# Kernel tuning notes

Hardware: AMD Instinct MI355X
Metric: run time of the kernel (lower is better)

Reference implementation:

```python
import jax, jax.numpy as jnp
import numpy as np

# Module constants (from source defaults)
RING = 256      # ring_len
D = 128         # slot_dim
IN = 64         # input_dim
SD = max(8, D // 3)  # sensory_dim = 42
K = 2           # gauss_k -> 2K+1 = 5 taps
TAU = 8.0       # gauss_tau
NC = 1000       # num_classes
B, T = 512, 512


def setup_inputs() -> dict:
    key = jax.random.key(0)
    ks = jax.random.split(key, 10)
    g = lambda k, shape, s=0.05: jax.random.normal(k, shape, jnp.float32) * s
    return {
        "x": jax.random.normal(ks[0], (B, T, IN), jnp.float32),
        "theta_ptr": jnp.array([37.0], jnp.float32),
        "w_proj": g(ks[1], (SD, IN)), "b_proj": jnp.zeros((SD,), jnp.float32),
        "w_ih": g(ks[2], (3 * SD, SD)), "w_hh": g(ks[3], (3 * SD, SD)),
        "b_ih": jnp.zeros((3 * SD,), jnp.float32), "b_hh": jnp.zeros((3 * SD,), jnp.float32),
        "w_bridge": g(ks[4], (D, SD)), "b_bridge": jnp.zeros((D,), jnp.float32),
        "w_jump": g(ks[5], (1, D)), "b_jump": jnp.zeros((1,), jnp.float32),
        "w_gate": g(ks[6], (1, D)), "b_gate": jnp.zeros((1,), jnp.float32),
        "w_cls": g(ks[7], (NC, D)), "b_cls": jnp.zeros((NC,), jnp.float32),
    }


def _kernel(ptr):
    """Gaussian soft window around a fractional ring pointer. ptr: [B] float."""
    offs = jnp.arange(-K, K + 1)
    base = jnp.floor(ptr)
    frac = ptr - base                               # [B]
    pos = jnp.mod(base.astype(jnp.int32)[:, None] + offs[None, :], RING)  # [B, 2K+1]
    d = offs.astype(ptr.dtype)[None, :] - frac[:, None]
    w = jax.nn.softmax(-(d * d) / TAU, axis=-1)     # [B, 2K+1]
    return pos, w


def reference(x, theta_ptr, w_proj, b_proj, w_ih, w_hh, b_ih, b_hh,
              w_bridge, b_bridge, w_jump, b_jump, w_gate, b_gate, w_cls, b_cls):
    Bn = x.shape[0]
    bidx = jnp.arange(Bn)
    ring0 = jnp.zeros((Bn, RING, D), x.dtype)
    h0 = jnp.zeros((Bn, SD), x.dtype)
    ptr0 = jnp.broadcast_to(jnp.mod(theta_ptr, float(RING)), (Bn,)).astype(x.dtype)

    def step(carry, xt):
        ring, h, ptr = carry
        # sensory path: Linear -> GRUCell -> bridge
        s = xt @ w_proj.T + b_proj
        gx = s @ w_ih.T + b_ih
        gh = h @ w_hh.T + b_hh
        rg = jax.nn.sigmoid(gx[:, :SD] + gh[:, :SD])
        zg = jax.nn.sigmoid(gx[:, SD:2 * SD] + gh[:, SD:2 * SD])
        ng = jnp.tanh(gx[:, 2 * SD:] + rg * gh[:, 2 * SD:])
        h = (1.0 - zg) * ng + zg * h
        u = jnp.tanh(h @ w_bridge.T + b_bridge)      # write vector [B, D]
        # soft-kernel read at current pointer
        pos, w = _kernel(ptr)
        r = jnp.einsum('bk,bkd->bd', w, ring[bidx[:, None], pos])
        # pointer jump target + gate, circ_lerp along shortest arc
        jump = jax.nn.sigmoid(r @ w_jump.T + b_jump)[:, 0] * RING
        gate = jax.nn.sigmoid(r @ w_gate.T + b_gate)[:, 0]
        delta = jnp.mod(jump - ptr + RING / 2.0, float(RING)) - RING / 2.0  # wrap_delta
        ptr = jnp.mod(ptr + gate * delta, float(RING))                      # circ_lerp
        # soft-kernel write at new pointer
        pos2, w2 = _kernel(ptr)
        ring = ring.at[bidx[:, None], pos2].add(w2[..., None] * u[:, None, :])
        return (ring, h, ptr), None

    (ring, h, ptr), _ = jax.lax.scan(step, (ring0, h0, ptr0), jnp.swapaxes(x, 0, 1))
    pos, w = _kernel(ptr)
    r = jnp.einsum('bk,bkd->bd', w, ring[bidx[:, None], pos])
    return r @ w_cls.T + b_cls
```

## Files before the change

### kernel.cpp

```cpp
#include <hip/hip_runtime.h>
#include <hip/hip_bf16.h>
#include <cstdint>

#define RINGN 256
#define DD    128
#define SDN   42
#define G3N   126
#define INN   64
#define BN    512
#define TN    512
#define NCN   1000
#define HS    44
#define GXS   128
#define BT    (BN * TN)
#define HSLOTS 32
#define GSLOTS 16

typedef float v2f __attribute__((ext_vector_type(2)));
typedef float4 __attribute__((may_alias)) f4ma;
typedef float2 __attribute__((may_alias)) f2ma;

__device__ __forceinline__ float sigm(float x)    { return 1.0f / (1.0f + __expf(-x)); }
__device__ __forceinline__ float tanhfast(float x){ float e = __expf(2.0f * x); return 1.0f - 2.0f / (e + 1.0f); }
__device__ __forceinline__ float wrap256(float x) { return x - 256.0f * floorf(x * 0.00390625f); }

__device__ __forceinline__ void taps_norm(float p, int* pos, float* w) {
  float base = floorf(p);
  float frac = p - base;
  int ib = (int)base;
  float e[5];
  float s = 0.0f;
#pragma unroll
  for (int k = 0; k < 5; k++) {
    float d = (float)(k - 2) - frac;
    e[k] = __expf(-(d * d) * 0.125f);
    s += e[k];
    pos[k] = (ib + k - 2) & 255;
  }
  float inv = 1.0f / s;
#pragma unroll
  for (int k = 0; k < 5; k++) w[k] = e[k] * inv;
}

template<int C>
__device__ __forceinline__ float dpp_add_step(float x) {
  int t = __builtin_amdgcn_update_dpp(0, __float_as_int(x), C, 0xf, 0xf, true);
  return x + __int_as_float(t);
}
__device__ __forceinline__ float wave_sum64(float x) {
  x = dpp_add_step<0x111>(x);
  x = dpp_add_step<0x112>(x);
  x = dpp_add_step<0x114>(x);
  x = dpp_add_step<0x118>(x);
  x = dpp_add_step<0x142>(x);
  x = dpp_add_step<0x143>(x);
  return __int_as_float(__builtin_amdgcn_readlane(__float_as_int(x), 63));
}

__global__ void prep_kernel(const float* __restrict__ w_ih, const float* __restrict__ w_proj,
                            const float* __restrict__ b_proj, const float* __restrict__ b_ih,
                            float* __restrict__ Wc, float* __restrict__ bc) {
  int idx = blockIdx.x * 256 + threadIdx.x;
  if (idx < G3N * INN) {
    int j = idx / INN, i = idx % INN;
    float a = 0.0f;
    for (int k = 0; k < SDN; k++) a += w_ih[j * SDN + k] * w_proj[k * INN + i];
    Wc[idx] = a;
  }
  if (idx < G3N) {
    float a = b_ih[idx];
    for (int k = 0; k < SDN; k++) a += w_ih[idx * SDN + k] * b_proj[k];
    bc[idx] = a;
  }
}

__global__ __launch_bounds__(256, 1)
void rec4_kernel(const float* __restrict__ x,
                 const float* __restrict__ Wc,
                 const float* __restrict__ bc,
                 const float* __restrict__ w_hh, const float* __restrict__ b_hh,
                 const float* __restrict__ w_bridge, const float* __restrict__ b_bridge,
                 const float* __restrict__ w_jump, const float* __restrict__ b_jump,
                 const float* __restrict__ w_gate, const float* __restrict__ b_gate,
                 const float* __restrict__ theta,
                 float* __restrict__ hbuf, float* __restrict__ ptrbuf) {
  const int tid = threadIdx.x;
  const int wid = tid >> 6;
  const int lane = tid & 63;
  const int b = blockIdx.x;

  __shared__ float2 JG[RINGN];
  __shared__ __align__(16) float h_ring[HSLOTS * HS];
  __shared__ __align__(16) float gx_ring[GSLOTS * GXS];
  __shared__ __align__(16) float xst[2 * INN];
  __shared__ float ringJ[TN];
  __shared__ float ringG[TN];
  __shared__ int flagH;
  __shared__ int done1;
  __shared__ int flagG;

  if (tid == 0) { flagH = 0; done1 = 0; flagG = 0; }
  __syncthreads();

  if (wid == 3) {
    const v2f* wc2 = (const v2f*)Wc;
    v2f Wr0[32], Wr1[32];
#pragma unroll
    for (int i = 0; i < 32; i++) {
      Wr0[i] = wc2[lane * 32 + i];
      Wr1[i] = (lane < 62) ? wc2[(64 + lane) * 32 + i] : (v2f){0.f, 0.f};
    }
    const float bcv0 = bc[lane];
    const float bcv1 = (lane < 62) ? bc[64 + lane] : 0.0f;

    const float* xb = x + (size_t)b * TN * INN;
    float xcur = xb[lane];
    float xnxt = xb[INN + lane];

    volatile int* fH = &flagH;
    volatile int* fG = &flagG;

    for (int t = 0; t < TN; t++) {
      if (t >= 12) {
        while (*fH < t - 12) __builtin_amdgcn_s_sleep(1);
      }
      float* xs = &xst[(t & 1) * INN];
      xs[lane] = xcur;
      __builtin_amdgcn_wave_barrier();
      asm volatile("" ::: "memory");
      const f2ma* xp = (const f2ma*)xs;
      v2f acc0 = (v2f){bcv0, 0.0f};
      v2f acc1 = (v2f){bcv1, 0.0f};
#pragma unroll
      for (int i = 0; i < 32; i++) {
        float2 xv = xp[i];
        v2f xr = (v2f){xv.x, xv.y};
        acc0 = __builtin_elementwise_fma(Wr0[i], xr, acc0);
        acc1 = __builtin_elementwise_fma(Wr1[i], xr, acc1);
      }
      float* slot = &gx_ring[(t & (GSLOTS - 1)) * GXS];
      slot[lane] = acc0.x + acc0.y;
      if (lane < 62) slot[64 + lane] = acc1.x + acc1.y;
      asm volatile("s_waitcnt lgkmcnt(0)" ::: "memory");
      if (lane == 0) *fG = t + 1;
      xcur = xnxt;
      if (t + 2 < TN) xnxt = xb[(size_t)(t + 2) * INN + lane];
    }
  } else if (wid == 0) {
    const int jj = (lane < SDN) ? lane : (SDN - 1);

    const v2f* whh2 = (const v2f*)w_hh;
    v2f Whr[21], Whz[21], Whn[21];
#pragma unroll
    for (int k = 0; k < 21; k++) {
      Whr[k] = whh2[jj * 21 + k];
      Whz[k] = whh2[(jj + SDN) * 21 + k];
      Whn[k] = whh2[(jj + 2 * SDN) * 21 + k];
    }
    const float bhr = b_hh[jj], bhz = b_hh[jj + SDN], bhn = b_hh[jj + 2 * SDN];

    v2f hv2[22];
#pragma unroll
    for (int k = 0; k < 22; k++) hv2[k] = (v2f){0.f, 0.f};
    float hprev = 0.0f;

    const int o0 = jj, o1 = SDN + jj, o2 = 2 * SDN + jj;
    float* hb = hbuf + (size_t)b * TN * HS;

    volatile int* fH = &flagH;
    volatile int* fC = &done1;
    volatile int* fG = &flagG;
    int seenG = 0;

    if (seenG < 1) { while ((seenG = *fG) < 1) __builtin_amdgcn_s_sleep(1); }
    asm volatile("" ::: "memory");
    float cu0 = gx_ring[o0], cu1 = gx_ring[o1], cu2 = gx_ring[o2];

    for (int t = 0; t < TN; t++) {
      if ((t & 7) == 0 && t >= HSLOTS) {
        while (*fC < t - 24) __builtin_amdgcn_s_sleep(1);
      }
      v2f ar = (v2f){bhr, 0.f}, az = (v2f){bhz, 0.f}, an = (v2f){bhn, 0.f};
#pragma unroll
      for (int k = 0; k < 21; k++) {
        v2f h2 = hv2[k];
        ar = __builtin_elementwise_fma(Whr[k], h2, ar);
        az = __builtin_elementwise_fma(Whz[k], h2, az);
        an = __builtin_elementwise_fma(Whn[k], h2, an);
      }
      float ghr = ar.x + ar.y, ghz = az.x + az.y, ghn = an.x + an.y;
      float rgate = sigm(cu0 + ghr);
      float zg = sigm(cu1 + ghz);
      float ng = tanhfast(cu2 + rgate * ghn);
      float hn = (1.0f - zg) * ng + zg * hprev;
      hprev = hn;

      float* slot = &h_ring[(t & (HSLOTS - 1)) * HS];
      if (lane < SDN) {
        slot[lane] = hn;
        hb[(size_t)t * HS + lane] = hn;
      }
      asm volatile("s_waitcnt lgkmcnt(0)" ::: "memory");
      if (lane == 0) *fH = t + 1;
      __builtin_amdgcn_wave_barrier();
      asm volatile("" ::: "memory");

#pragma unroll
      for (int k4 = 0; k4 < 11; k4++) {
        float4 v = *(const f4ma*)(&slot[k4 * 4]);
        hv2[2 * k4]     = (v2f){v.x, v.y};
        hv2[2 * k4 + 1] = (v2f){v.z, v.w};
      }

      if (t + 1 < TN) {
        if (seenG < t + 2) {
          while ((seenG = *fG) < t + 2) __builtin_amdgcn_s_sleep(1);
        }
        asm volatile("" ::: "memory");
        const float* gs = &gx_ring[((t + 1) & (GSLOTS - 1)) * GXS];
        cu0 = gs[o0]; cu1 = gs[o1]; cu2 = gs[o2];
      }
    }
  } else if (wid == 1) {
    const int r1 = lane + 64;
    const v2f* wb2 = (const v2f*)w_bridge;
    v2f Wb0[21], Wb1[21];
#pragma unroll
    for (int k = 0; k < 21; k++) {
      Wb0[k] = wb2[lane * 21 + k];
      Wb1[k] = wb2[r1 * 21 + k];
    }
    const float bb0 = b_bridge[lane], bb1 = b_bridge[r1];
    const float wj0 = w_jump[lane], wj1 = w_jump[r1];
    const float wg0 = w_gate[lane], wg1 = w_gate[r1];

    volatile int* fH = &flagH;
    volatile int* fC = &done1;
    int seenH = 0;

    for (int t = 0; t < TN; t++) {
      if (seenH <= t) {
        while ((seenH = *fH) <= t) __builtin_amdgcn_s_sleep(1);
      }
      asm volatile("" ::: "memory");
      const float* slot = &h_ring[(t & (HSLOTS - 1)) * HS];
      v2f hw[22];
#pragma unroll
      for (int k4 = 0; k4 < 11; k4++) {
        float4 v = *(const f4ma*)(&slot[k4 * 4]);
        hw[2 * k4]     = (v2f){v.x, v.y};
        hw[2 * k4 + 1] = (v2f){v.z, v.w};
      }
      v2f a0 = (v2f){bb0, 0.f}, a1 = (v2f){bb1, 0.f};
#pragma unroll
      for (int k = 0; k < 21; k++) {
        v2f h2 = hw[k];
        a0 = __builtin_elementwise_fma(Wb0[k], h2, a0);
        a1 = __builtin_elementwise_fma(Wb1[k], h2, a1);
      }
      float u0 = tanhfast(a0.x + a0.y);
      float u1 = tanhfast(a1.x + a1.y);

      float pjs = wave_sum64(u0 * wj0 + u1 * wj1);
      float pgs = wave_sum64(u0 * wg0 + u1 * wg1);

      if (lane == 0) { ringJ[t] = pjs; ringG[t] = pgs; }
      asm volatile("s_waitcnt lgkmcnt(0)" ::: "memory");
      if (lane == 0) *fC = t + 1;
    }
  } else {
    for (int i = lane; i < RINGN; i += 64) JG[i] = make_float2(0.f, 0.f);
    __builtin_amdgcn_wave_barrier();
    asm volatile("" ::: "memory");

    const float bj = b_jump[0], bg = b_gate[0];
    float ptr = wrap256(theta[0]);
    float* pb = ptrbuf + (size_t)b * TN;

    float wk[5]; float2 Vk[5];
    {
      int posk[5];
      taps_norm(ptr, posk, wk);
#pragma unroll
      for (int k = 0; k < 5; k++) Vk[k] = JG[posk[k]];
    }
    float pjprev = 0.f, pgprev = 0.f, S2prev = 0.f;
    volatile int* rdy = &done1;
    int seen = 0;

    for (int t = 0; t < TN; t++) {
      float dotJ = 0.f, dotG = 0.f;
#pragma unroll
      for (int k = 0; k < 5; k++) { dotJ += wk[k] * Vk[k].x; dotG += wk[k] * Vk[k].y; }
      float Jv = fmaf(pjprev, S2prev, dotJ);
      float Gv = fmaf(pgprev, S2prev, dotG);
      float jump = 256.0f * sigm(Jv + bj);
      float gate = sigm(Gv + bg);
      float delta = wrap256(jump - ptr + 128.0f) - 128.0f;
      float ptr2 = wrap256(ptr + gate * delta);

      float tbase = floorf(ptr2);
      float frac = ptr2 - tbase;
      int ib = (int)tbase;
      float e2[5], ssum = 0.f; int pos2[5];
#pragma unroll
      for (int k = 0; k < 5; k++) {
        float d = (float)(k - 2) - frac;
        e2[k] = __expf(-(d * d) * 0.125f);
        ssum += e2[k];
        pos2[k] = (ib + k - 2) & 255;
      }
      float inv2 = 1.0f / ssum;
      float2 Vk2[5];
#pragma unroll
      for (int k = 0; k < 5; k++) Vk2[k] = JG[pos2[k]];
      float w2n[5], S2 = 0.f;
#pragma unroll
      for (int k = 0; k < 5; k++) { w2n[k] = e2[k] * inv2; S2 = fmaf(w2n[k], w2n[k], S2); }
      if (lane == 0) pb[t] = ptr2;

      if (seen <= t) {
        while ((seen = *rdy) <= t) __builtin_amdgcn_s_sleep(1);
      }
      asm volatile("" ::: "memory");
      float pjs = ringJ[t];
      float pgs = ringG[t];

      int p2sel = pos2[0]; float w2sel = w2n[0];
#pragma unroll
      for (int k = 1; k < 5; k++) {
        if (lane == k) { p2sel = pos2[k]; w2sel = w2n[k]; }
      }
      if (lane < 5) {
        atomicAdd(&JG[p2sel].x, w2sel * pjs);
        atomicAdd(&JG[p2sel].y, w2sel * pgs);
      }

#pragma unroll
      for (int k = 0; k < 5; k++) { wk[k] = w2n[k]; Vk[k] = Vk2[k]; }
      S2prev = S2; pjprev = pjs; pgprev = pgs; ptr = ptr2;
    }
  }
}

__global__ __launch_bounds__(64)
void rfinal_kernel(const float* __restrict__ hbuf, const float* __restrict__ ptrbuf,
                   const float* __restrict__ w_bridge, const float* __restrict__ b_bridge,
                   float* __restrict__ rbuf) {
  const int b = blockIdx.x;
  const int chunk = blockIdx.y;
  const int lane = threadIdx.x;
  const int t0 = chunk * 128;
  const int r1 = lane + 64;

  __shared__ float c_lds[128];

  const float* pb = ptrbuf + (size_t)b * TN;
  float ptrf = pb[TN - 1];
  int posf[5]; float wf[5];
  taps_norm(ptrf, posf, wf);

#pragma unroll
  for (int rr = 0; rr < 2; rr++) {
    int tt = rr * 64 + lane;
    int p2[5]; float w2[5];
    taps_norm(pb[t0 + tt], p2, w2);
    float c = 0.0f;
#pragma unroll
    for (int k = 0; k < 5; k++)
#pragma unroll
      for (int k2 = 0; k2 < 5; k2++)
        c += (posf[k] == p2[k2]) ? wf[k] * w2[k2] : 0.0f;
    c_lds[tt] = c;
  }
  __builtin_amdgcn_wave_barrier();
  asm volatile("" ::: "memory");

  const v2f* wb2 = (const v2f*)w_bridge;
  v2f Wb0[21], Wb1[21];
#pragma unroll
  for (int k = 0; k < 21; k++) { Wb0[k] = wb2[lane * 21 + k]; Wb1[k] = wb2[r1 * 21 + k]; }
  float bb0 = b_bridge[lane], bb1 = b_bridge[r1];

  float racc0 = 0.0f, racc1 = 0.0f;
  for (int tt = 0; tt < 128; tt++) {
    float ct = c_lds[tt];
    if (ct != 0.0f) {
      const f4ma* hp = (const f4ma*)(hbuf + ((size_t)b * TN + t0 + tt) * HS);
      v2f hx[22];
#pragma unroll
      for (int i = 0; i < 11; i++) {
        float4 v = hp[i];
        hx[2 * i]     = (v2f){v.x, v.y};
        hx[2 * i + 1] = (v2f){v.z, v.w};
      }
      v2f a0 = (v2f){bb0, 0.f}, a1 = (v2f){bb1, 0.f};
#pragma unroll
      for (int k = 0; k < 21; k++) {
        a0 = __builtin_elementwise_fma(Wb0[k], hx[k], a0);
        a1 = __builtin_elementwise_fma(Wb1[k], hx[k], a1);
      }
      racc0 += ct * tanhfast(a0.x + a0.y);
      racc1 += ct * tanhfast(a1.x + a1.y);
    }
  }
  atomicAdd(&rbuf[b * DD + lane], racc0);
  atomicAdd(&rbuf[b * DD + 64 + lane], racc1);
}

__global__ __launch_bounds__(256)
void cls_kernel(const float* __restrict__ rbuf, const float* __restrict__ w_cls,
                const float* __restrict__ b_cls, float* __restrict__ out) {
  const int b0 = blockIdx.x * 4;
  const int tid = threadIdx.x;
  __shared__ __align__(16) float r[4 * DD];
  for (int i = tid; i < 4 * DD; i += 256) r[i] = rbuf[(size_t)b0 * DD + i];
  __syncthreads();

  for (int c = tid; c < NCN; c += 256) {
    float bcv = b_cls[c];
    float a0 = bcv, a1 = bcv, a2 = bcv, a3 = bcv;
    const float* wrow = &w_cls[(size_t)c * DD];
#pragma unroll
    for (int d4 = 0; d4 < DD / 4; d4++) {
      float4 wv = *reinterpret_cast<const float4*>(&wrow[d4 * 4]);
      float4 r0 = *(const f4ma*)(&r[0 * DD + d4 * 4]);
      float4 r1 = *(const f4ma*)(&r[1 * DD + d4 * 4]);
      float4 r2 = *(const f4ma*)(&r[2 * DD + d4 * 4]);
      float4 r3 = *(const f4ma*)(&r[3 * DD + d4 * 4]);
      a0 += wv.x * r0.x + wv.y * r0.y + wv.z * r0.z + wv.w * r0.w;
      a1 += wv.x * r1.x + wv.y * r1.y + wv.z * r1.z + wv.w * r1.w;
      a2 += wv.x * r2.x + wv.y * r2.y + wv.z * r2.z + wv.w * r2.w;
      a3 += wv.x * r3.x + wv.y * r3.y + wv.z * r3.z + wv.w * r3.w;
    }
    out[(size_t)(b0 + 0) * NCN + c] = a0;
    out[(size_t)(b0 + 1) * NCN + c] = a1;
    out[(size_t)(b0 + 2) * NCN + c] = a2;
    out[(size_t)(b0 + 3) * NCN + c] = a3;
  }
}

extern "C" void kernel_launch(void* const* d_in, const int* in_sizes, int n_in,
                              void* d_out, int out_size, void* d_ws, size_t ws_size,
                              hipStream_t stream) {
  const float* x        = (const float*)d_in[0];
  const float* theta    = (const float*)d_in[1];
  const float* w_proj   = (const float*)d_in[2];
  const float* b_proj   = (const float*)d_in[3];
  const float* w_ih     = (const float*)d_in[4];
  const float* w_hh     = (const float*)d_in[5];
  const float* b_ih     = (const float*)d_in[6];
  const float* b_hh     = (const float*)d_in[7];
  const float* w_bridge = (const float*)d_in[8];
  const float* b_bridge = (const float*)d_in[9];
  const float* w_jump   = (const float*)d_in[10];
  const float* b_jump   = (const float*)d_in[11];
  const float* w_gate   = (const float*)d_in[12];
  const float* b_gate   = (const float*)d_in[13];
  const float* w_cls    = (const float*)d_in[14];
  const float* b_cls    = (const float*)d_in[15];
  float* out = (float*)d_out;

  char* ws = (char*)d_ws;
  size_t off = 0;
  float* hbuf   = (float*)(ws + off); off += (size_t)BN * TN * HS * 4;
  float* ptrbuf = (float*)(ws + off); off += (size_t)BN * TN * 4;
  float* rbuf   = (float*)(ws + off); off += (size_t)BN * DD * 4;
  float* Wc     = (float*)(ws + off); off += (((size_t)G3N * INN * 4 + 255) & ~(size_t)255);
  float* bc     = (float*)(ws + off); off += 512;

  hipMemsetAsync(rbuf, 0, (size_t)BN * DD * 4, stream);
  prep_kernel<<<32, 256, 0, stream>>>(w_ih, w_proj, b_proj, b_ih, Wc, bc);
  rec4_kernel<<<BN, 256, 0, stream>>>(x, Wc, bc, w_hh, b_hh, w_bridge, b_bridge,
                                      w_jump, b_jump, w_gate, b_gate, theta, hbuf, ptrbuf);
  dim3 gfin(BN, 4);
  rfinal_kernel<<<gfin, 64, 0, stream>>>(hbuf, ptrbuf, w_bridge, b_bridge, rbuf);
  cls_kernel<<<BN / 4, 256, 0, stream>>>(rbuf, w_cls, b_cls, out);
}
```

Measured before the change: 563.1 us.

## Stage projection weights in LDS, deepen x prefetch, replace LDS atomics with stores

The projection wave no longer holds the 126x64 projection matrix in 128 VGPRs. It stages the matrix in padded shared memory with a stride of 66 to avoid bank conflicts and reads it every step. It also prefetches x four steps ahead instead of two, and polls the producer flag only every fourth step. In the pointer wave, the LDS atomic adds on the jump/gate table become plain stores of the previously read value plus the update, which assumes the five tap positions are distinct. The aim is to relieve register pressure and trim sync overhead, at the cost of extra LDS traffic in the inner loop.

```diff
diff --git a/kernel.cpp b/kernel.cpp
--- a/kernel.cpp
+++ b/kernel.cpp
@@ -15,6 +15,7 @@
 #define BT    (BN * TN)
 #define HSLOTS 32
 #define GSLOTS 16
+#define WCS   66
 
 typedef float v2f __attribute__((ext_vector_type(2)));
 typedef float4 __attribute__((may_alias)) f4ma;
@@ -93,6 +94,7 @@
   __shared__ __align__(16) float h_ring[HSLOTS * HS];
   __shared__ __align__(16) float gx_ring[GSLOTS * GXS];
   __shared__ __align__(16) float xst[2 * INN];
+  __shared__ __align__(16) float WcS66[G3N * WCS];
   __shared__ float ringJ[TN];
   __shared__ float ringG[TN];
   __shared__ int flagH;
@@ -103,25 +105,29 @@
   __syncthreads();
 
   if (wid == 3) {
-    const v2f* wc2 = (const v2f*)Wc;
-    v2f Wr0[32], Wr1[32];
-#pragma unroll
-    for (int i = 0; i < 32; i++) {
-      Wr0[i] = wc2[lane * 32 + i];
-      Wr1[i] = (lane < 62) ? wc2[(64 + lane) * 32 + i] : (v2f){0.f, 0.f};
-    }
+    for (int idx = lane; idx < G3N * INN; idx += 64) {
+      WcS66[(idx >> 6) * WCS + (idx & 63)] = Wc[idx];
+    }
+    asm volatile("s_waitcnt lgkmcnt(0)" ::: "memory");
+    __builtin_amdgcn_wave_barrier();
+
+    const int c1 = (lane < 62) ? (64 + lane) : 125;
     const float bcv0 = bc[lane];
     const float bcv1 = (lane < 62) ? bc[64 + lane] : 0.0f;
+    const f2ma* w0 = (const f2ma*)&WcS66[lane * WCS];
+    const f2ma* w1 = (const f2ma*)&WcS66[c1 * WCS];
 
     const float* xb = x + (size_t)b * TN * INN;
     float xcur = xb[lane];
-    float xnxt = xb[INN + lane];
+    float xn1 = xb[INN + lane];
+    float xn2 = xb[2 * INN + lane];
+    float xn3 = xb[3 * INN + lane];
 
     volatile int* fH = &flagH;
     volatile int* fG = &flagG;
 
     for (int t = 0; t < TN; t++) {
-      if (t >= 12) {
+      if ((t & 3) == 0 && t >= 12) {
         while (*fH < t - 12) __builtin_amdgcn_s_sleep(1);
       }
       float* xs = &xst[(t & 1) * INN];
@@ -135,16 +141,18 @@
       for (int i = 0; i < 32; i++) {
         float2 xv = xp[i];
         v2f xr = (v2f){xv.x, xv.y};
-        acc0 = __builtin_elementwise_fma(Wr0[i], xr, acc0);
-        acc1 = __builtin_elementwise_fma(Wr1[i], xr, acc1);
+        float2 wv0 = w0[i];
+        float2 wv1 = w1[i];
+        acc0 = __builtin_elementwise_fma((v2f){wv0.x, wv0.y}, xr, acc0);
+        acc1 = __builtin_elementwise_fma((v2f){wv1.x, wv1.y}, xr, acc1);
       }
       float* slot = &gx_ring[(t & (GSLOTS - 1)) * GXS];
       slot[lane] = acc0.x + acc0.y;
       if (lane < 62) slot[64 + lane] = acc1.x + acc1.y;
       asm volatile("s_waitcnt lgkmcnt(0)" ::: "memory");
       if (lane == 0) *fG = t + 1;
-      xcur = xnxt;
-      if (t + 2 < TN) xnxt = xb[(size_t)(t + 2) * INN + lane];
+      xcur = xn1; xn1 = xn2; xn2 = xn3;
+      if (t + 4 < TN) xn3 = xb[(size_t)(t + 4) * INN + lane];
     }
   } else if (wid == 0) {
     const int jj = (lane < SDN) ? lane : (SDN - 1);
@@ -326,14 +334,13 @@
       float pjs = ringJ[t];
       float pgs = ringG[t];
 
-      int p2sel = pos2[0]; float w2sel = w2n[0];
+      int p2sel = pos2[0]; float w2sel = w2n[0]; float2 vsel = Vk2[0];
 #pragma unroll
       for (int k = 1; k < 5; k++) {
-        if (lane == k) { p2sel = pos2[k]; w2sel = w2n[k]; }
+        if (lane == k) { p2sel = pos2[k]; w2sel = w2n[k]; vsel = Vk2[k]; }
       }
       if (lane < 5) {
-        atomicAdd(&JG[p2sel].x, w2sel * pjs);
-        atomicAdd(&JG[p2sel].y, w2sel * pgs);
+        JG[p2sel] = make_float2(vsel.x + w2sel * pjs, vsel.y + w2sel * pgs);
       }
 
 #pragma unroll
```

Measured after the change: 669.8 us. 18.9% more time.
